# Performance work log

Measured on AMD Instinct MI355X. Metric: run time of the kernel, lower is better.

## Reference

```python
import jax, jax.numpy as jnp
import numpy as np

K = 8192  # particles
T = 4096  # timesteps
LOG2PI = float(np.log(2.0 * np.pi))


def _normal_logpdf(x, mu):
    # Normal(mu, 1).log_prob(x)
    return -0.5 * (x - mu) ** 2 - 0.5 * LOG2PI


def setup_inputs() -> dict:
    key = jax.random.key(0)
    k1, k2, k3, k4 = jax.random.split(key, 4)
    x = jax.random.normal(k1, (T,), dtype=jnp.float32)          # observations
    w0 = jax.random.normal(k2, (K,), dtype=jnp.float32)          # Pw=N(0,1) samples
    z = jax.random.normal(k3, (K, T), dtype=jnp.float32)         # Qz=N(0,1) samples
    u = jax.random.uniform(k4, (T, K), dtype=jnp.float32)        # resampling uniforms
    return {"x": x, "w0": w0, "z": z, "u": u}


def reference(x, w0, z, u):
    # Precompute terms that the torch code computes once before the loop.
    log_Qz = _normal_logpdf(z, 0.0)                 # [K, T]  q.Qz().log_prob(z)
    log_PxGz = _normal_logpdf(x[None, :], z)        # [K, T]  p.PxGz(z).log_prob(x)
    delta = log_PxGz - log_Qz                       # [K, T]
    logK = jnp.log(jnp.asarray(K, dtype=z.dtype))

    def step(w, inp):
        z_t, d_t, u_t = inp                         # each [K]
        # log_ws = p.PzGw(w).log_prob(z_t) + log_PxGz_t - log_Qz_t
        log_ws = _normal_logpdf(z_t, w) + d_t       # [K]
        lme = jax.nn.logsumexp(log_ws) - logK       # logmeanexp over particles
        # Categorical(logits=log_ws).sample([K]) via inverse-CDF with uniforms
        cdf = jnp.cumsum(jax.nn.softmax(log_ws))    # [K]
        idx = jnp.clip(jnp.searchsorted(cdf, u_t), 0, K - 1)  # [K]
        return w[idx], lme                          # resample: w = w[idx]

    _, res = jax.lax.scan(step, w0, (z.T, delta.T, u))  # scan over T timesteps
    return jnp.sum(res)
```

## Files before the change

### kernel.cpp

```cpp
#include <hip/hip_runtime.h>
#include <math.h>

#define KP 8192
#define TSTEPS 4096
#define BLOCK 1024
#define PT 8
#define NWAVES 16
#define NBUCK 8192
#define NBF 8192.0f
#define INV_NB (1.0f / 8192.0f)

template <int CTRL, int RM>
__device__ __forceinline__ float dpp_add_f(float x) {
  int s = __builtin_amdgcn_update_dpp(0, __float_as_int(x), CTRL, RM, 0xF, false);
  return x + __int_as_float(s);
}
template <int CTRL, int RM>
__device__ __forceinline__ int dpp_max_i(int x) {
  int s = __builtin_amdgcn_update_dpp(0, x, CTRL, RM, 0xF, false);
  return x > s ? x : s;
}
__device__ __forceinline__ float wscan64_add(float x) {
  x = dpp_add_f<0x111, 0xF>(x); x = dpp_add_f<0x112, 0xF>(x);
  x = dpp_add_f<0x114, 0xF>(x); x = dpp_add_f<0x118, 0xF>(x);
  x = dpp_add_f<0x142, 0xA>(x); x = dpp_add_f<0x143, 0xC>(x);
  return x;
}
__device__ __forceinline__ int wscan64_max(int x) {
  x = dpp_max_i<0x111, 0xF>(x); x = dpp_max_i<0x112, 0xF>(x);
  x = dpp_max_i<0x114, 0xF>(x); x = dpp_max_i<0x118, 0xF>(x);
  x = dpp_max_i<0x142, 0xA>(x); x = dpp_max_i<0x143, 0xC>(x);
  return x;
}
__device__ __forceinline__ float rscan16_add(float x) {
  x = dpp_add_f<0x111, 0xF>(x); x = dpp_add_f<0x112, 0xF>(x);
  x = dpp_add_f<0x114, 0xF>(x); x = dpp_add_f<0x118, 0xF>(x);
  return x;
}
__device__ __forceinline__ int rscan16_max(int x) {
  x = dpp_max_i<0x111, 0xF>(x); x = dpp_max_i<0x112, 0xF>(x);
  x = dpp_max_i<0x114, 0xF>(x); x = dpp_max_i<0x118, 0xF>(x);
  return x;
}
__device__ __forceinline__ float readlane_f(float v, int l) {
  return __int_as_float(__builtin_amdgcn_readlane(__float_as_int(v), l));
}

__global__ void transpose_k(const float* __restrict__ in, float* __restrict__ out) {
  __shared__ float tile[32][33];
  const int c0 = blockIdx.x * 32;
  const int r0 = blockIdx.y * 32;
  const int tx = threadIdx.x;
  const int ty = threadIdx.y;
#pragma unroll
  for (int i = 0; i < 32; i += 8)
    tile[ty + i][tx] = in[(size_t)(r0 + ty + i) * TSTEPS + c0 + tx];
  __syncthreads();
#pragma unroll
  for (int i = 0; i < 32; i += 8)
    out[(size_t)(c0 + ty + i) * KP + r0 + tx] = tile[tx][ty + i];
}

template <bool ZTRANS>
__global__ __launch_bounds__(BLOCK) void smc_scan(const float* __restrict__ x,
                                                  const float* __restrict__ w0,
                                                  const float* __restrict__ zsrc,
                                                  const float* __restrict__ u,
                                                  float* __restrict__ out) {
  extern __shared__ float sm[];
  float* wbufA = sm;
  float* wbufB = sm + KP;
  float* cdf_s = sm + 2 * KP;
  float* cend  = cdf_s + KP;
  float* red   = cend + BLOCK;
  int*   redi  = (int*)(red + NWAVES);
  int*   bcI   = redi + NWAVES;
  int*   L_s   = bcI + 4;

  const int tid = threadIdx.x;
  const int lane = tid & 63;
  const int wid = tid >> 6;
  const int kbase = tid * PT;

  float* wcur = wbufA;
  float* wnxt = wbufB;

  for (int i = tid; i < NBUCK; i += BLOCK) L_s[i] = 0;
  if (tid == 0) L_s[NBUCK] = KP - 1;

  float wv[PT];
  {
    float4 a = *(const float4*)(w0 + kbase);
    float4 b = *(const float4*)(w0 + kbase + 4);
    wv[0] = a.x; wv[1] = a.y; wv[2] = a.z; wv[3] = a.w;
    wv[4] = b.x; wv[5] = b.y; wv[6] = b.z; wv[7] = b.w;
    *(float4*)(wcur + kbase) = a;
    *(float4*)(wcur + kbase + 4) = b;
  }
  __syncthreads();

  float zn[PT], un[PT];
  float xt_next = x[0];
  if (ZTRANS) {
    float4 a = *(const float4*)(zsrc + kbase);
    float4 b = *(const float4*)(zsrc + kbase + 4);
    zn[0] = a.x; zn[1] = a.y; zn[2] = a.z; zn[3] = a.w;
    zn[4] = b.x; zn[5] = b.y; zn[6] = b.z; zn[7] = b.w;
  } else {
#pragma unroll
    for (int j = 0; j < PT; ++j) zn[j] = zsrc[(size_t)(kbase + j) * TSTEPS];
  }
  {
    float4 a = *(const float4*)(u + kbase);
    float4 b = *(const float4*)(u + kbase + 4);
    un[0] = a.x; un[1] = a.y; un[2] = a.z; un[3] = a.w;
    un[4] = b.x; un[5] = b.y; un[6] = b.z; un[7] = b.w;
  }

  float acc = 0.f;

  for (int t = 0; t < TSTEPS; ++t) {
    float zv[PT], uv[PT];
#pragma unroll
    for (int j = 0; j < PT; ++j) { zv[j] = zn[j]; uv[j] = un[j]; }
    const float xt = xt_next;

    if (t + 1 < TSTEPS) {
      xt_next = x[t + 1];
      if (ZTRANS) {
        float4 a = *(const float4*)(zsrc + (size_t)(t + 1) * KP + kbase);
        float4 b = *(const float4*)(zsrc + (size_t)(t + 1) * KP + kbase + 4);
        zn[0] = a.x; zn[1] = a.y; zn[2] = a.z; zn[3] = a.w;
        zn[4] = b.x; zn[5] = b.y; zn[6] = b.z; zn[7] = b.w;
      } else {
#pragma unroll
        for (int j = 0; j < PT; ++j)
          zn[j] = zsrc[(size_t)(kbase + j) * TSTEPS + t + 1];
      }
      float4 a = *(const float4*)(u + (size_t)(t + 1) * KP + kbase);
      float4 b = *(const float4*)(u + (size_t)(t + 1) * KP + kbase + 4);
      un[0] = a.x; un[1] = a.y; un[2] = a.z; un[3] = a.w;
      un[4] = b.x; un[5] = b.y; un[6] = b.z; un[7] = b.w;
    }

    float s[PT];
    float run = 0.f;
#pragma unroll
    for (int j = 0; j < PT; ++j) {
      float d = zv[j] - wv[j];
      float lw = fmaf(xt, zv[j], -0.5f * d * d);
      run += __expf(lw);
      s[j] = run;
    }
    const float wincl = wscan64_add(run);
    const float wexcl = wincl - run;
    if (lane == 63) red[wid] = wincl;
    __syncthreads();

    float v16 = rscan16_add(red[lane & 15]);
    const float total = readlane_f(v16, 15);
    const float wpre = wid ? readlane_f(v16, wid - 1) : 0.f;
    const float base = wpre + wexcl;
    const float invT = 1.0f / total;

    float cvn[PT];
#pragma unroll
    for (int j = 0; j < PT; ++j) cvn[j] = (base + s[j]) * invT;
    {
      float4 a, b;
      a.x = cvn[0]; a.y = cvn[1]; a.z = cvn[2]; a.w = cvn[3];
      b.x = cvn[4]; b.y = cvn[5]; b.z = cvn[6]; b.w = cvn[7];
      *(float4*)(cdf_s + kbase) = a;
      *(float4*)(cdf_s + kbase + 4) = b;
    }
    cend[tid] = cvn[PT - 1];
    if (tid == BLOCK - 1) bcI[0] = (int)(cvn[PT - 1] * NBF);
    {
      int4 z4; z4.x = z4.y = z4.z = z4.w = 0;
      *(int4*)(L_s + kbase) = z4;
      *(int4*)(L_s + kbase + 4) = z4;
    }
    if (tid == 0)
      acc += __logf(total) - 9.0109133472792886f
             - 0.5f * (1.8378770664093453f + xt * xt);
    __syncthreads();

    {
      const float cprev = tid ? cend[tid - 1] : 0.f;
      int flo = (int)(cprev * NBF);
#pragma unroll
      for (int j = 0; j < PT; ++j) {
        int fhi = (int)(cvn[j] * NBF);
        if (fhi > NBUCK - 1) fhi = NBUCK - 1;
        if (fhi > flo) L_s[flo + 1] = kbase + j;
        flo = fhi;
      }
    }
    __syncthreads();

    int4 ra = *(const int4*)(L_s + kbase);
    int4 rb = *(const int4*)(L_s + kbase + 4);
    int c1 = max(ra.x, ra.y);
    int c2 = max(c1, ra.z);
    int c3 = max(c2, ra.w);
    int c4 = max(c3, rb.x);
    int c5 = max(c4, rb.y);
    int c6 = max(c5, rb.z);
    int c7 = max(c6, rb.w);
    const int mincl = wscan64_max(c7);
    int mexcl = __shfl_up(mincl, 1);
    if (lane == 0) mexcl = 0;
    if (lane == 63) redi[wid] = mincl;
    __syncthreads();

    {
      int mv = rscan16_max(redi[lane & 15]);
      const int crosspre = wid ? __builtin_amdgcn_readlane(mv, wid - 1) : 0;
      const int fhiLast = bcI[0];
      int m = max(crosspre, mexcl);
      int4 oa, ob;
      m = max(m, ra.x); oa.x = (kbase + 0 > fhiLast) ? (KP - 1) : m;
      m = max(m, ra.y); oa.y = (kbase + 1 > fhiLast) ? (KP - 1) : m;
      m = max(m, ra.z); oa.z = (kbase + 2 > fhiLast) ? (KP - 1) : m;
      m = max(m, ra.w); oa.w = (kbase + 3 > fhiLast) ? (KP - 1) : m;
      m = max(m, rb.x); ob.x = (kbase + 4 > fhiLast) ? (KP - 1) : m;
      m = max(m, rb.y); ob.y = (kbase + 5 > fhiLast) ? (KP - 1) : m;
      m = max(m, rb.z); ob.z = (kbase + 6 > fhiLast) ? (KP - 1) : m;
      m = max(m, rb.w); ob.w = (kbase + 7 > fhiLast) ? (KP - 1) : m;
      *(int4*)(L_s + kbase) = oa;
      *(int4*)(L_s + kbase + 4) = ob;
    }
    __syncthreads();

    int lo[PT], len[PT];
    float tg[PT], fr0[PT];
#pragma unroll
    for (int j = 0; j < PT; ++j) {
      tg[j] = uv[j];
      const float fb = uv[j] * NBF;
      int b = (int)fb;
      b = min(b, NBUCK - 1);
      fr0[j] = fb - (float)b;
      const int i0 = L_s[b];
      const int i1 = L_s[b + 1];
      lo[j] = i0;
      len[j] = i1 - i0;
    }
    int anylen = 0;
#pragma unroll
    for (int j = 0; j < PT; ++j) {
      int off = (int)(fr0[j] * (float)len[j]);
      off = min(off, len[j] - 1);
      off = max(off, 0);
      const float c = cdf_s[lo[j] + off];
      const bool adv = (c < tg[j]) & (len[j] > 0);
      lo[j] = adv ? lo[j] + off + 1 : lo[j];
      len[j] = adv ? len[j] - off - 1 : (len[j] > 0 ? off : 0);
      anylen |= len[j];
    }
    while (anylen) {
      anylen = 0;
#pragma unroll
      for (int j = 0; j < PT; ++j) {
        const int half = len[j] >> 1;
        const float c = cdf_s[lo[j] + half];
        const bool adv = (c < tg[j]) & (len[j] > 0);
        lo[j] = adv ? lo[j] + half + 1 : lo[j];
        len[j] = adv ? len[j] - half - 1 : half;
        anylen |= len[j];
      }
    }

    float nw[PT];
#pragma unroll
    for (int j = 0; j < PT; ++j) nw[j] = wcur[lo[j]];
    {
      float4 a, b;
      a.x = nw[0]; a.y = nw[1]; a.z = nw[2]; a.w = nw[3];
      b.x = nw[4]; b.y = nw[5]; b.z = nw[6]; b.w = nw[7];
      *(float4*)(wnxt + kbase) = a;
      *(float4*)(wnxt + kbase + 4) = b;
    }
#pragma unroll
    for (int j = 0; j < PT; ++j) wv[j] = nw[j];
    float* tmp = wcur; wcur = wnxt; wnxt = tmp;
  }

  if (tid == 0) out[0] = acc;
}

extern "C" void kernel_launch(void* const* d_in, const int* in_sizes, int n_in,
                              void* d_out, int out_size, void* d_ws, size_t ws_size,
                              hipStream_t stream) {
  const float* x = (const float*)d_in[0];
  const float* w0 = (const float*)d_in[1];
  const float* z = (const float*)d_in[2];
  const float* u = (const float*)d_in[3];
  float* out = (float*)d_out;

  const size_t zbytes = (size_t)KP * TSTEPS * sizeof(float);
  const size_t shmem =
      (size_t)(3 * KP + BLOCK + NWAVES + NWAVES + 4 + NBUCK + 1) * sizeof(float);

  if (ws_size >= zbytes) {
    float* zT = (float*)d_ws;
    transpose_k<<<dim3(TSTEPS / 32, KP / 32), dim3(32, 8), 0, stream>>>(z, zT);
    smc_scan<true><<<1, BLOCK, shmem, stream>>>(x, w0, zT, u, out);
  } else {
    smc_scan<false><<<1, BLOCK, shmem, stream>>>(x, w0, z, u, out);
  }
}
```

Measured before the change: 20.86 ms.

## Presort resampling uniforms in parallel and invert search direction in sequential scan

Adds a fully parallel pre-pass kernel that sorts each timestep's uniforms with a bucket counting sort plus insertion sort, storing the sorted values, per-particle ranks and bucket offsets. The sequential single-block scan then searches each particle's CDF value in the sorted uniforms rather than searching each uniform in the CDF, and builds the ancestor map with tagged atomicMax plus a max-scan. The point is to move per-step bucket construction over the CDF off the serial critical path. The cost is extra workspace (sorted u, ranks, offsets) and extra global traffic per step, and the fallback search path was also simplified.

```diff
diff --git a/kernel.cpp b/kernel.cpp
--- a/kernel.cpp
+++ b/kernel.cpp
@@ -9,11 +9,17 @@
 #define NBUCK 8192
 #define NBF 8192.0f
 #define INV_NB (1.0f / 8192.0f)
+#define RS_LU 8208
 
 template <int CTRL, int RM>
 __device__ __forceinline__ float dpp_add_f(float x) {
   int s = __builtin_amdgcn_update_dpp(0, __float_as_int(x), CTRL, RM, 0xF, false);
   return x + __int_as_float(s);
+}
+template <int CTRL, int RM>
+__device__ __forceinline__ int dpp_add_i(int x) {
+  int s = __builtin_amdgcn_update_dpp(0, x, CTRL, RM, 0xF, false);
+  return x + s;
 }
 template <int CTRL, int RM>
 __device__ __forceinline__ int dpp_max_i(int x) {
@@ -26,6 +32,12 @@
   x = dpp_add_f<0x142, 0xA>(x); x = dpp_add_f<0x143, 0xC>(x);
   return x;
 }
+__device__ __forceinline__ int wscan64_addi(int x) {
+  x = dpp_add_i<0x111, 0xF>(x); x = dpp_add_i<0x112, 0xF>(x);
+  x = dpp_add_i<0x114, 0xF>(x); x = dpp_add_i<0x118, 0xF>(x);
+  x = dpp_add_i<0x142, 0xA>(x); x = dpp_add_i<0x143, 0xC>(x);
+  return x;
+}
 __device__ __forceinline__ int wscan64_max(int x) {
   x = dpp_max_i<0x111, 0xF>(x); x = dpp_max_i<0x112, 0xF>(x);
   x = dpp_max_i<0x114, 0xF>(x); x = dpp_max_i<0x118, 0xF>(x);
@@ -35,6 +47,11 @@
 __device__ __forceinline__ float rscan16_add(float x) {
   x = dpp_add_f<0x111, 0xF>(x); x = dpp_add_f<0x112, 0xF>(x);
   x = dpp_add_f<0x114, 0xF>(x); x = dpp_add_f<0x118, 0xF>(x);
+  return x;
+}
+__device__ __forceinline__ int rscan16_addi(int x) {
+  x = dpp_add_i<0x111, 0xF>(x); x = dpp_add_i<0x112, 0xF>(x);
+  x = dpp_add_i<0x114, 0xF>(x); x = dpp_add_i<0x118, 0xF>(x);
   return x;
 }
 __device__ __forceinline__ int rscan16_max(int x) {
@@ -59,6 +76,311 @@
 #pragma unroll
   for (int i = 0; i < 32; i += 8)
     out[(size_t)(c0 + ty + i) * KP + r0 + tx] = tile[tx][ty + i];
+}
+
+__global__ __launch_bounds__(BLOCK) void sortu_k(const float* __restrict__ u,
+                                                 float* __restrict__ su,
+                                                 unsigned short* __restrict__ rnk,
+                                                 unsigned short* __restrict__ lu) {
+  __shared__ int hist[NBUCK];
+  __shared__ float sval[KP];
+  __shared__ unsigned short sidx[KP];
+  __shared__ int redi[NWAVES];
+  const int t = blockIdx.x;
+  const int tid = threadIdx.x;
+  const int lane = tid & 63;
+  const int wid = tid >> 6;
+  const int kbase = tid * PT;
+
+  float uv[PT];
+  {
+    float4 a = *(const float4*)(u + (size_t)t * KP + kbase);
+    float4 b = *(const float4*)(u + (size_t)t * KP + kbase + 4);
+    uv[0] = a.x; uv[1] = a.y; uv[2] = a.z; uv[3] = a.w;
+    uv[4] = b.x; uv[5] = b.y; uv[6] = b.z; uv[7] = b.w;
+  }
+  int bj[PT];
+#pragma unroll
+  for (int j = 0; j < PT; ++j) {
+    int b = (int)(uv[j] * NBF);
+    bj[j] = b > NBUCK - 1 ? NBUCK - 1 : b;
+  }
+  {
+    int4 z4; z4.x = z4.y = z4.z = z4.w = 0;
+    *(int4*)(hist + kbase) = z4;
+    *(int4*)(hist + kbase + 4) = z4;
+  }
+  __syncthreads();
+#pragma unroll
+  for (int j = 0; j < PT; ++j) atomicAdd(&hist[bj[j]], 1);
+  __syncthreads();
+
+  int4 ha = *(const int4*)(hist + kbase);
+  int4 hb = *(const int4*)(hist + kbase + 4);
+  int c0 = ha.x, c1 = c0 + ha.y, c2 = c1 + ha.z, c3 = c2 + ha.w;
+  int c4 = c3 + hb.x, c5 = c4 + hb.y, c6 = c5 + hb.z, c7 = c6 + hb.w;
+  int wincl = wscan64_addi(c7);
+  int wexcl = wincl - c7;
+  if (lane == 63) redi[wid] = wincl;
+  __syncthreads();
+  int v16 = rscan16_addi(redi[lane & 15]);
+  int cp = wid ? __builtin_amdgcn_readlane(v16, wid - 1) : 0;
+  int base = cp + wexcl;
+  int ex[PT];
+  ex[0] = base; ex[1] = base + c0; ex[2] = base + c1; ex[3] = base + c2;
+  ex[4] = base + c3; ex[5] = base + c4; ex[6] = base + c5; ex[7] = base + c6;
+  {
+    int p0 = (ex[0] & 0xffff) | (ex[1] << 16);
+    int p1 = (ex[2] & 0xffff) | (ex[3] << 16);
+    int p2 = (ex[4] & 0xffff) | (ex[5] << 16);
+    int p3 = (ex[6] & 0xffff) | (ex[7] << 16);
+    int4 pk; pk.x = p0; pk.y = p1; pk.z = p2; pk.w = p3;
+    *(int4*)(lu + (size_t)t * RS_LU + kbase) = pk;
+  }
+  {
+    int4 pa; pa.x = ex[0]; pa.y = ex[1]; pa.z = ex[2]; pa.w = ex[3];
+    int4 pb; pb.x = ex[4]; pb.y = ex[5]; pb.z = ex[6]; pb.w = ex[7];
+    *(int4*)(hist + kbase) = pa;
+    *(int4*)(hist + kbase + 4) = pb;
+  }
+  __syncthreads();
+#pragma unroll
+  for (int j = 0; j < PT; ++j) {
+    int pos = atomicAdd(&hist[bj[j]], 1);
+    sval[pos] = uv[j];
+    sidx[pos] = (unsigned short)(kbase + j);
+  }
+  __syncthreads();
+  for (int bb = tid; bb < NBUCK; bb += BLOCK) {
+    int s0 = bb ? hist[bb - 1] : 0;
+    int e0 = hist[bb];
+    for (int m = s0 + 1; m < e0; ++m) {
+      float v = sval[m];
+      unsigned short ix = sidx[m];
+      int p = m - 1;
+      while (p >= s0 && sval[p] > v) {
+        sval[p + 1] = sval[p];
+        sidx[p + 1] = sidx[p];
+        --p;
+      }
+      sval[p + 1] = v;
+      sidx[p + 1] = ix;
+    }
+  }
+  __syncthreads();
+  {
+    float4 a, b;
+    a.x = sval[kbase + 0]; a.y = sval[kbase + 1]; a.z = sval[kbase + 2]; a.w = sval[kbase + 3];
+    b.x = sval[kbase + 4]; b.y = sval[kbase + 5]; b.z = sval[kbase + 6]; b.w = sval[kbase + 7];
+    *(float4*)(su + (size_t)t * KP + kbase) = a;
+    *(float4*)(su + (size_t)t * KP + kbase + 4) = b;
+  }
+#pragma unroll
+  for (int j = 0; j < PT; ++j)
+    rnk[(size_t)t * KP + sidx[kbase + j]] = (unsigned short)(kbase + j);
+}
+
+__global__ __launch_bounds__(BLOCK) void smc_scan2(const float* __restrict__ x,
+                                                   const float* __restrict__ w0,
+                                                   const float* __restrict__ zsrc,
+                                                   const float* __restrict__ su_g,
+                                                   const unsigned short* __restrict__ rk_g,
+                                                   const unsigned short* __restrict__ lu_g,
+                                                   float* __restrict__ out) {
+  extern __shared__ float sm[];
+  float* wbufA = sm;
+  float* wbufB = sm + KP;
+  float* su_s = sm + 2 * KP;
+  int* P_s = (int*)(su_s + KP + 8);
+  unsigned short* Lu_s = (unsigned short*)(P_s + KP + 8);
+  float* redF = (float*)(Lu_s + KP + 16);
+  int* redI = (int*)(redF + NWAVES);
+  int* bcI = redI + NWAVES;
+
+  const int tid = threadIdx.x;
+  const int lane = tid & 63;
+  const int wid = tid >> 6;
+  const int kbase = tid * PT;
+
+  float* wcur = wbufA;
+  float* wnxt = wbufB;
+
+  for (int i = tid; i < KP + 8; i += BLOCK) P_s[i] = 0;
+  if (tid == 0) Lu_s[KP] = (unsigned short)KP;
+
+  float wv[PT];
+  {
+    float4 a = *(const float4*)(w0 + kbase);
+    float4 b = *(const float4*)(w0 + kbase + 4);
+    wv[0] = a.x; wv[1] = a.y; wv[2] = a.z; wv[3] = a.w;
+    wv[4] = b.x; wv[5] = b.y; wv[6] = b.z; wv[7] = b.w;
+    *(float4*)(wcur + kbase) = a;
+    *(float4*)(wcur + kbase + 4) = b;
+  }
+
+  float4 zna, znb, sna, snb;
+  int4 lun, rkn;
+  float xt_next = x[0];
+  zna = *(const float4*)(zsrc + kbase);
+  znb = *(const float4*)(zsrc + kbase + 4);
+  sna = *(const float4*)(su_g + kbase);
+  snb = *(const float4*)(su_g + kbase + 4);
+  lun = *(const int4*)(lu_g + kbase);
+  rkn = *(const int4*)(rk_g + kbase);
+  __syncthreads();
+
+  float acc = 0.f;
+
+  for (int t = 0; t < TSTEPS; ++t) {
+    *(float4*)(su_s + kbase) = sna;
+    *(float4*)(su_s + kbase + 4) = snb;
+    *(int4*)(Lu_s + kbase) = lun;
+    float zv[PT];
+    zv[0] = zna.x; zv[1] = zna.y; zv[2] = zna.z; zv[3] = zna.w;
+    zv[4] = znb.x; zv[5] = znb.y; zv[6] = znb.z; zv[7] = znb.w;
+    const int4 rkc = rkn;
+    const float xt = xt_next;
+
+    if (t + 1 < TSTEPS) {
+      xt_next = x[t + 1];
+      const size_t ro = (size_t)(t + 1) * KP + kbase;
+      zna = *(const float4*)(zsrc + ro);
+      znb = *(const float4*)(zsrc + ro + 4);
+      sna = *(const float4*)(su_g + ro);
+      snb = *(const float4*)(su_g + ro + 4);
+      lun = *(const int4*)(lu_g + (size_t)(t + 1) * RS_LU + kbase);
+      rkn = *(const int4*)(rk_g + ro);
+    }
+
+    float s[PT];
+    float run = 0.f;
+#pragma unroll
+    for (int j = 0; j < PT; ++j) {
+      float d = zv[j] - wv[j];
+      float lw = fmaf(xt, zv[j], -0.5f * d * d);
+      run += __expf(lw);
+      s[j] = run;
+    }
+    const float wincl = wscan64_add(run);
+    const float wexcl = wincl - run;
+    if (lane == 63) redF[wid] = wincl;
+    __syncthreads();
+
+    float v16 = rscan16_add(redF[lane & 15]);
+    const float total = readlane_f(v16, 15);
+    const float wpre = wid ? readlane_f(v16, wid - 1) : 0.f;
+    const float base = wpre + wexcl;
+    const float invT = 1.0f / total;
+    if (tid == 0)
+      acc += __logf(total) - 9.0109133472792886f
+             - 0.5f * (1.8378770664093453f + xt * xt);
+    float cvn[PT];
+#pragma unroll
+    for (int j = 0; j < PT; ++j) cvn[j] = (base + s[j]) * invT;
+
+    int lo[PT], len[PT];
+    int anylen = 0;
+#pragma unroll
+    for (int j = 0; j < PT; ++j) {
+      float fb = cvn[j] * NBF;
+      int b = (int)fb;
+      b = b > NBUCK - 1 ? NBUCK - 1 : b;
+      b = b < 0 ? 0 : b;
+      const int l = Lu_s[b];
+      const int h = Lu_s[b + 1];
+      lo[j] = l;
+      len[j] = h - l;
+      anylen |= len[j];
+    }
+    while (anylen) {
+      anylen = 0;
+#pragma unroll
+      for (int j = 0; j < PT; ++j) {
+        const int half = len[j] >> 1;
+        const float v = su_s[lo[j] + half];
+        const bool adv = (v <= cvn[j]) & (len[j] > 0);
+        lo[j] = adv ? lo[j] + half + 1 : lo[j];
+        len[j] = adv ? len[j] - half - 1 : half;
+        anylen |= len[j];
+      }
+    }
+
+    const int tagv = (t + 1) << 14;
+    {
+      int pr = __shfl_up(lo[PT - 1], 1);
+      if (lane == 0) pr = 0x7fffffff;
+#pragma unroll
+      for (int j = 0; j < PT; ++j) {
+        if (lo[j] > pr) atomicMax(&P_s[pr], tagv | (kbase + j));
+        pr = lo[j];
+      }
+      if (lane == 63 && tid != BLOCK - 1)
+        atomicMax(&P_s[lo[PT - 1]], tagv | (kbase + PT));
+      if (tid == BLOCK - 1) bcI[0] = lo[PT - 1];
+    }
+    __syncthreads();
+
+    int4 pa = *(const int4*)(P_s + kbase);
+    int4 pb = *(const int4*)(P_s + kbase + 4);
+    const int e0 = pa.x >= tagv ? (pa.x & 16383) : 0;
+    const int e1 = pa.y >= tagv ? (pa.y & 16383) : 0;
+    const int e2 = pa.z >= tagv ? (pa.z & 16383) : 0;
+    const int e3 = pa.w >= tagv ? (pa.w & 16383) : 0;
+    const int e4 = pb.x >= tagv ? (pb.x & 16383) : 0;
+    const int e5 = pb.y >= tagv ? (pb.y & 16383) : 0;
+    const int e6 = pb.z >= tagv ? (pb.z & 16383) : 0;
+    const int e7 = pb.w >= tagv ? (pb.w & 16383) : 0;
+    int m1 = max(e0, e1), m2 = max(m1, e2), m3 = max(m2, e3);
+    int m4 = max(m3, e4), m5 = max(m4, e5), m6 = max(m5, e6), m7 = max(m6, e7);
+    const int mincl = wscan64_max(m7);
+    int mexcl = __shfl_up(mincl, 1);
+    if (lane == 0) mexcl = 0;
+    if (lane == 63) redI[wid] = mincl;
+    __syncthreads();
+
+    {
+      int mv = rscan16_max(redI[lane & 15]);
+      const int crosspre = wid ? __builtin_amdgcn_readlane(mv, wid - 1) : 0;
+      const int Rlast = bcI[0];
+      int m = max(crosspre, mexcl);
+      int4 oa, ob;
+      m = max(m, e0); oa.x = tagv | ((kbase + 0 >= Rlast) ? (KP - 1) : m);
+      m = max(m, e1); oa.y = tagv | ((kbase + 1 >= Rlast) ? (KP - 1) : m);
+      m = max(m, e2); oa.z = tagv | ((kbase + 2 >= Rlast) ? (KP - 1) : m);
+      m = max(m, e3); oa.w = tagv | ((kbase + 3 >= Rlast) ? (KP - 1) : m);
+      m = max(m, e4); ob.x = tagv | ((kbase + 4 >= Rlast) ? (KP - 1) : m);
+      m = max(m, e5); ob.y = tagv | ((kbase + 5 >= Rlast) ? (KP - 1) : m);
+      m = max(m, e6); ob.z = tagv | ((kbase + 6 >= Rlast) ? (KP - 1) : m);
+      m = max(m, e7); ob.w = tagv | ((kbase + 7 >= Rlast) ? (KP - 1) : m);
+      *(int4*)(P_s + kbase) = oa;
+      *(int4*)(P_s + kbase + 4) = ob;
+    }
+    __syncthreads();
+
+    {
+      int r[PT];
+      r[0] = rkc.x & 0xffff; r[1] = (rkc.x >> 16) & 0xffff;
+      r[2] = rkc.y & 0xffff; r[3] = (rkc.y >> 16) & 0xffff;
+      r[4] = rkc.z & 0xffff; r[5] = (rkc.z >> 16) & 0xffff;
+      r[6] = rkc.w & 0xffff; r[7] = (rkc.w >> 16) & 0xffff;
+      int idxv[PT];
+#pragma unroll
+      for (int j = 0; j < PT; ++j) idxv[j] = P_s[r[j]] & 16383;
+      float nw[PT];
+#pragma unroll
+      for (int j = 0; j < PT; ++j) nw[j] = wcur[idxv[j]];
+      float4 a, b;
+      a.x = nw[0]; a.y = nw[1]; a.z = nw[2]; a.w = nw[3];
+      b.x = nw[4]; b.y = nw[5]; b.z = nw[6]; b.w = nw[7];
+      *(float4*)(wnxt + kbase) = a;
+      *(float4*)(wnxt + kbase + 4) = b;
+#pragma unroll
+      for (int j = 0; j < PT; ++j) wv[j] = nw[j];
+    }
+    float* tmp = wcur; wcur = wnxt; wnxt = tmp;
+  }
+
+  if (tid == 0) out[0] = acc;
 }
 
 template <bool ZTRANS>
@@ -71,11 +393,11 @@
   float* wbufA = sm;
   float* wbufB = sm + KP;
   float* cdf_s = sm + 2 * KP;
-  float* cend  = cdf_s + KP;
-  float* red   = cend + BLOCK;
-  int*   redi  = (int*)(red + NWAVES);
-  int*   bcI   = redi + NWAVES;
-  int*   L_s   = bcI + 4;
+  float* cend = cdf_s + KP;
+  float* red = cend + BLOCK;
+  int* redi = (int*)(red + NWAVES);
+  int* bcI = redi + NWAVES;
+  int* L_s = bcI + 4;
 
   const int tid = threadIdx.x;
   const int lane = tid & 63;
@@ -233,29 +555,18 @@
     __syncthreads();
 
     int lo[PT], len[PT];
-    float tg[PT], fr0[PT];
+    float tg[PT];
+    int anylen = 0;
 #pragma unroll
     for (int j = 0; j < PT; ++j) {
       tg[j] = uv[j];
       const float fb = uv[j] * NBF;
       int b = (int)fb;
       b = min(b, NBUCK - 1);
-      fr0[j] = fb - (float)b;
       const int i0 = L_s[b];
       const int i1 = L_s[b + 1];
       lo[j] = i0;
       len[j] = i1 - i0;
-    }
-    int anylen = 0;
-#pragma unroll
-    for (int j = 0; j < PT; ++j) {
-      int off = (int)(fr0[j] * (float)len[j]);
-      off = min(off, len[j] - 1);
-      off = max(off, 0);
-      const float c = cdf_s[lo[j] + off];
-      const bool adv = (c < tg[j]) & (len[j] > 0);
-      lo[j] = adv ? lo[j] + off + 1 : lo[j];
-      len[j] = adv ? len[j] - off - 1 : (len[j] > 0 ? off : 0);
       anylen |= len[j];
     }
     while (anylen) {
@@ -298,15 +609,37 @@
   const float* u = (const float*)d_in[3];
   float* out = (float*)d_out;
 
-  const size_t zbytes = (size_t)KP * TSTEPS * sizeof(float);
-  const size_t shmem =
-      (size_t)(3 * KP + BLOCK + NWAVES + NWAVES + 4 + NBUCK + 1) * sizeof(float);
-
-  if (ws_size >= zbytes) {
-    float* zT = (float*)d_ws;
+  const size_t SZ_ZT = (size_t)KP * TSTEPS * sizeof(float);
+  const size_t OFF_SU = SZ_ZT;
+  const size_t SZ_SU = SZ_ZT;
+  const size_t OFF_RK = OFF_SU + SZ_SU;
+  const size_t SZ_RK = (size_t)KP * TSTEPS * 2;
+  const size_t OFF_LU = OFF_RK + SZ_RK;
+  const size_t SZ_LU = (size_t)TSTEPS * RS_LU * 2;
+  const size_t FULL = OFF_LU + SZ_LU;
+
+  if (ws_size >= FULL) {
+    char* ws = (char*)d_ws;
+    float* zT = (float*)ws;
+    float* su = (float*)(ws + OFF_SU);
+    unsigned short* rk = (unsigned short*)(ws + OFF_RK);
+    unsigned short* lu = (unsigned short*)(ws + OFF_LU);
     transpose_k<<<dim3(TSTEPS / 32, KP / 32), dim3(32, 8), 0, stream>>>(z, zT);
-    smc_scan<true><<<1, BLOCK, shmem, stream>>>(x, w0, zT, u, out);
+    sortu_k<<<TSTEPS, BLOCK, 0, stream>>>(u, su, rk, lu);
+    const size_t shmem2 =
+        ((size_t)KP * 2 + (KP + 8)  + (KP + 8) ) * sizeof(float) +
+        (size_t)(KP + 16) * sizeof(unsigned short) +
+        (size_t)(NWAVES) * sizeof(float) + (size_t)(NWAVES + 4) * sizeof(int);
+    smc_scan2<<<1, BLOCK, shmem2, stream>>>(x, w0, zT, su, rk, lu, out);
   } else {
-    smc_scan<false><<<1, BLOCK, shmem, stream>>>(x, w0, z, u, out);
-  }
-}
+    const size_t shmem =
+        (size_t)(3 * KP + BLOCK + NWAVES + NWAVES + 4 + NBUCK + 1) * sizeof(float);
+    if (ws_size >= SZ_ZT) {
+      float* zT = (float*)d_ws;
+      transpose_k<<<dim3(TSTEPS / 32, KP / 32), dim3(32, 8), 0, stream>>>(z, zT);
+      smc_scan<true><<<1, BLOCK, shmem, stream>>>(x, w0, zT, u, out);
+    } else {
+      smc_scan<false><<<1, BLOCK, shmem, stream>>>(x, w0, z, u, out);
+    }
+  }
+}
```

Result: slower. 34.54 ms (+65.6%).
